# Performance work log

Measured on AMD Instinct MI355X. Metric: run time of the kernel, lower is better.

The kernel has to match this reference:

```python
import jax, jax.numpy as jnp
import numpy as np

D_MODEL = 256
N_HEADS = 8
D_HEAD = D_MODEL // N_HEADS
B = 65536
LN_EPS = 1e-5


def setup_inputs() -> dict:
    key = jax.random.key(0)
    ks = jax.random.split(key, 6)
    s = 1.0 / np.sqrt(D_MODEL)
    x = jax.random.normal(ks[0], (B, D_MODEL), dtype=jnp.float32)
    Wq = jax.random.normal(ks[1], (D_MODEL, D_MODEL), dtype=jnp.float32) * s
    Wk = jax.random.normal(ks[2], (D_MODEL, D_MODEL), dtype=jnp.float32) * s
    Wv = jax.random.normal(ks[3], (D_MODEL, D_MODEL), dtype=jnp.float32) * s
    Wout = jax.random.normal(ks[4], (D_MODEL, D_MODEL), dtype=jnp.float32) * s
    b_out = jnp.zeros((D_MODEL,), dtype=jnp.float32)
    # L initialized to identity per head (matches nn.init.eye_) plus tiny noise
    L = jnp.broadcast_to(jnp.eye(D_HEAD, dtype=jnp.float32), (N_HEADS, D_HEAD, D_HEAD)) \
        + 0.01 * jax.random.normal(ks[5], (N_HEADS, D_HEAD, D_HEAD), dtype=jnp.float32)
    gamma = jnp.ones((D_MODEL,), dtype=jnp.float32)
    beta = jnp.zeros((D_MODEL,), dtype=jnp.float32)
    return {"x": x, "Wq": Wq, "Wk": Wk, "Wv": Wv, "Wout": Wout,
            "b_out": b_out, "L": L, "gamma": gamma, "beta": beta}


def reference(x, Wq, Wk, Wv, Wout, b_out, L, gamma, beta):
    b = x.shape[0]
    # projections; view as [B, H, d_head]
    Q = (x @ Wq).reshape(b, N_HEADS, D_HEAD)
    K = (x @ Wk).reshape(b, N_HEADS, D_HEAD)
    V = (x @ Wv).reshape(b, N_HEADS, D_HEAD)
    # pairwise head differences: [B, Hq, Hk, d_head]
    diff = Q[:, :, None, :] - K[:, None, :, :]
    # per-key-head learned metric transform: L indexed by key head
    diff_t = jnp.einsum('bqkd,kdf->bqkf', diff, L)
    sq_dist = jnp.sum(diff_t * diff_t, axis=-1)            # [B, Hq, Hk]
    attn = jax.nn.softmax(-sq_dist / jnp.sqrt(jnp.float32(D_HEAD)), axis=2)
    out = jnp.einsum('bqk,bkd->bqd', attn, V).reshape(b, D_MODEL)
    out = out @ Wout + b_out
    h = out + x
    # LayerNorm over last dim
    mu = jnp.mean(h, axis=-1, keepdims=True)
    var = jnp.mean((h - mu) ** 2, axis=-1, keepdims=True)
    return (h - mu) * jax.lax.rsqrt(var + LN_EPS) * gamma + beta
```

## Files before the change

kernel.cpp:

```cpp
#include <hip/hip_runtime.h>


typedef __bf16 bf16x8 __attribute__((ext_vector_type(8)));
typedef float  f32x4  __attribute__((ext_vector_type(4)));
typedef int    i32x4  __attribute__((ext_vector_type(4)));
typedef unsigned short u16;

__device__ __forceinline__ float bf2f(u16 u){
  unsigned int x = ((unsigned int)u) << 16;
  return __builtin_bit_cast(float, x);
}
__device__ __forceinline__ u16 f2bf(float f){
  unsigned int u = __builtin_bit_cast(unsigned int, f);
  u += 0x7FFFu + ((u >> 16) & 1u);
  return (u16)(u >> 16);
}
__device__ __forceinline__ unsigned int pk2(float lo, float hi){
  return ((unsigned int)f2bf(hi) << 16) | (unsigned int)f2bf(lo);
}
__device__ __forceinline__ bf16x8 ldfrag(const u16* p){
  return __builtin_bit_cast(bf16x8, *(const i32x4*)p);
}

#define LROW 264
#define HROW 260

__global__ __launch_bounds__(256) void geo_prep(
    const float* __restrict__ Wq, const float* __restrict__ Wk,
    const float* __restrict__ Wv, const float* __restrict__ Wout,
    const float* __restrict__ L, u16* __restrict__ ws)
{
  u16* Wd    = ws;
  u16* WvT   = ws + 524288;
  u16* WoutT = ws + 589824;
  const int b = blockIdx.x, t = threadIdx.x;

  if (b < 64){
    const int q = b >> 3, k = b & 7;
    __shared__ float dwb[256][33];
    __shared__ float Lk[32][33];
    for (int i = 0; i < 4; ++i){
      int idx = t + i*256;
      Lk[idx >> 5][idx & 31] = L[k*1024 + idx];
    }
    {
      const int c = t;
      const float* wqp = Wq + c*256 + q*32;
      const float* wkp = Wk + c*256 + k*32;
      #pragma unroll
      for (int j = 0; j < 8; ++j){
        f32x4 a  = *(const f32x4*)(wqp + j*4);
        f32x4 bb = *(const f32x4*)(wkp + j*4);
        #pragma unroll
        for (int p = 0; p < 4; ++p) dwb[c][j*4 + p] = a[p] - bb[p];
      }
    }
    __syncthreads();
    const int c = t;
    float wreg[32];
    #pragma unroll
    for (int d = 0; d < 32; ++d) wreg[d] = dwb[c][d];
    for (int f = 0; f < 32; ++f){
      float s = 0.f;
      #pragma unroll
      for (int d = 0; d < 32; ++d) s = fmaf(wreg[d], Lk[d][f], s);
      Wd[(size_t)(q*256 + k*32 + f)*256 + c] = f2bf(s);
    }
  } else {
    const int bb  = b - 64;
    const float* src = (bb < 16) ? Wv  : Wout;
    u16*         dst = (bb < 16) ? WvT : WoutT;
    const int tile = bb & 15;
    const int tr = tile >> 2, tc = tile & 3;
    __shared__ float tlf[64][68];
    {
      const int row = t >> 2, cs = (t & 3)*16;
      #pragma unroll
      for (int j = 0; j < 4; ++j){
        f32x4 v = *(const f32x4*)(src + (size_t)(tr*64 + row)*256 + tc*64 + cs + j*4);
        #pragma unroll
        for (int p = 0; p < 4; ++p) tlf[row][cs + j*4 + p] = v[p];
      }
    }
    __syncthreads();
    {
      const int n = t >> 2, cs = (t & 3)*16;
      float us[16];
      #pragma unroll
      for (int j = 0; j < 16; ++j) us[j] = tlf[cs + j][n];
      #pragma unroll
      for (int h = 0; h < 2; ++h){
        i32x4 o;
        #pragma unroll
        for (int p = 0; p < 4; ++p)
          o[p] = (int)pk2(us[h*8 + 2*p], us[h*8 + 2*p + 1]);
        *(i32x4*)(dst + (size_t)(tc*64 + n)*256 + tr*64 + cs + h*8) = o;
      }
    }
  }
}

__global__ __launch_bounds__(512) void geo_fused(
    const float* __restrict__ x,   const u16* __restrict__ Wd,
    const u16* __restrict__ WvT,   const u16* __restrict__ WoutT,
    const float* __restrict__ b_out, const float* __restrict__ gamma,
    const float* __restrict__ beta,  float* __restrict__ out)
{
  __shared__ __align__(16) char pool[125952];
  u16  (*xs)[LROW]   = (u16 (*)[LROW])(pool);
  u16  (*Vs)[LROW]   = (u16 (*)[LROW])(pool + 33792);
  u16  (*ao)[LROW]   = (u16 (*)[LROW])(pool + 67584);
  float (*sqs)[8][12] = (float (*)[8][12])(pool + 101376);
  float (*hs)[HROW]  = (float (*)[HROW])(pool);

  const int t    = threadIdx.x;
  const int lane = t & 63;
  const int w    = t >> 6;
  const int l15  = lane & 15;
  const int quad = lane >> 4;
  const long rowbase = (long)blockIdx.x * 64;

  {
    const int r  = t >> 3;
    const int c0 = (t & 7) * 32;
    const float* src = x + (rowbase + r)*256 + c0;
    unsigned int words[16];
    #pragma unroll
    for (int j = 0; j < 8; ++j){
      f32x4 v = *(const f32x4*)(src + j*4);
      words[j*2    ] = pk2(v[0], v[1]);
      words[j*2 + 1] = pk2(v[2], v[3]);
    }
    #pragma unroll
    for (int qd = 0; qd < 4; ++qd){
      i32x4 o;
      #pragma unroll
      for (int p = 0; p < 4; ++p) o[p] = (int)words[qd*4 + p];
      *(i32x4*)&xs[r][c0 + qd*8] = o;
    }
  }
  __syncthreads();

  {
    f32x4 acc[4][2];
    #pragma unroll
    for (int mt = 0; mt < 4; ++mt)
      #pragma unroll
      for (int nt = 0; nt < 2; ++nt) acc[mt][nt] = f32x4{0.f,0.f,0.f,0.f};
    #pragma unroll
    for (int kk = 0; kk < 8; ++kk){
      const int c0 = kk*32 + quad*8;
      bf16x8 a[4], bfr[2];
      #pragma unroll
      for (int mt = 0; mt < 4; ++mt) a[mt] = ldfrag(&xs[mt*16 + l15][c0]);
      #pragma unroll
      for (int nt = 0; nt < 2; ++nt){
        const int n = w*32 + nt*16 + l15;
        bfr[nt] = __builtin_bit_cast(bf16x8, *(const i32x4*)(WvT + (size_t)n*256 + c0));
      }
      #pragma unroll
      for (int mt = 0; mt < 4; ++mt)
        #pragma unroll
        for (int nt = 0; nt < 2; ++nt)
          acc[mt][nt] = __builtin_amdgcn_mfma_f32_16x16x32_bf16(a[mt], bfr[nt], acc[mt][nt], 0, 0, 0);
    }
    #pragma unroll
    for (int mt = 0; mt < 4; ++mt)
      #pragma unroll
      for (int nt = 0; nt < 2; ++nt){
        const int col = w*32 + nt*16 + l15;
        #pragma unroll
        for (int reg = 0; reg < 4; ++reg)
          Vs[mt*16 + quad*4 + reg][col] = f2bf(acc[mt][nt][reg]);
      }
  }

  {
    #pragma unroll
    for (int kp = 0; kp < 4; ++kp){
      f32x4 acc[2][2][4];
      #pragma unroll
      for (int k2 = 0; k2 < 2; ++k2)
        #pragma unroll
        for (int mt = 0; mt < 2; ++mt)
          #pragma unroll
          for (int nt = 0; nt < 4; ++nt) acc[k2][mt][nt] = f32x4{0.f,0.f,0.f,0.f};
      #pragma unroll
      for (int kk = 0; kk < 8; ++kk){
        const int c0 = kk*32 + quad*8;
        bf16x8 bfr[4];
        #pragma unroll
        for (int nt = 0; nt < 4; ++nt) bfr[nt] = ldfrag(&xs[nt*16 + l15][c0]);
        bf16x8 a[2][2];
        #pragma unroll
        for (int k2 = 0; k2 < 2; ++k2)
          #pragma unroll
          for (int mt = 0; mt < 2; ++mt){
            const int m = w*256 + (kp*2 + k2)*32 + mt*16 + l15;
            a[k2][mt] = __builtin_bit_cast(bf16x8, *(const i32x4*)(Wd + (size_t)m*256 + c0));
          }
        #pragma unroll
        for (int k2 = 0; k2 < 2; ++k2)
          #pragma unroll
          for (int mt = 0; mt < 2; ++mt)
            #pragma unroll
            for (int nt = 0; nt < 4; ++nt)
              acc[k2][mt][nt] = __builtin_amdgcn_mfma_f32_16x16x32_bf16(a[k2][mt], bfr[nt], acc[k2][mt][nt], 0, 0, 0);
      }
      #pragma unroll
      for (int k2 = 0; k2 < 2; ++k2){
        const int k = kp*2 + k2;
        #pragma unroll
        for (int nt = 0; nt < 4; ++nt){
          float s = 0.f;
          #pragma unroll
          for (int mt = 0; mt < 2; ++mt)
            #pragma unroll
            for (int reg = 0; reg < 4; ++reg){
              float d = acc[k2][mt][nt][reg];
              s = fmaf(d, d, s);
            }
          s += __shfl_xor(s, 16);
          s += __shfl_xor(s, 32);
          if (quad == 0) sqs[nt*16 + l15][w][k] = s;
        }
      }
    }
  }
  __syncthreads();

  {
    const int r = t >> 3, q = t & 7;
    float lg[8];
    #pragma unroll
    for (int k = 0; k < 8; ++k) lg[k] = sqs[r][q][k] * -0.17677669529663687f;
    float mx = lg[0];
    #pragma unroll
    for (int k = 1; k < 8; ++k) mx = fmaxf(mx, lg[k]);
    float e[8], sum = 0.f;
    #pragma unroll
    for (int k = 0; k < 8; ++k){ e[k] = __expf(lg[k] - mx); sum += e[k]; }
    const float inv = 1.0f / sum;
    #pragma unroll
    for (int k = 0; k < 8; ++k) e[k] *= inv;

    #pragma unroll
    for (int dc = 0; dc < 4; ++dc){
      const int d0 = dc*8;
      float o[8] = {0.f,0.f,0.f,0.f,0.f,0.f,0.f,0.f};
      #pragma unroll
      for (int k = 0; k < 8; ++k){
        i32x4 v = *(const i32x4*)&Vs[r][k*32 + d0];
        const float a = e[k];
        #pragma unroll
        for (int p = 0; p < 4; ++p){
          unsigned int u = (unsigned int)v[p];
          o[2*p    ] = fmaf(a, __builtin_bit_cast(float, u << 16),          o[2*p    ]);
          o[2*p + 1] = fmaf(a, __builtin_bit_cast(float, u & 0xFFFF0000u),  o[2*p + 1]);
        }
      }
      i32x4 pkv;
      #pragma unroll
      for (int p = 0; p < 4; ++p)
        pkv[p] = (int)pk2(o[2*p], o[2*p + 1]);
      *(i32x4*)&ao[r][q*32 + d0] = pkv;
    }
  }
  __syncthreads();

  {
    f32x4 acc[4][2];
    #pragma unroll
    for (int mt = 0; mt < 4; ++mt)
      #pragma unroll
      for (int nt = 0; nt < 2; ++nt) acc[mt][nt] = f32x4{0.f,0.f,0.f,0.f};
    #pragma unroll
    for (int kk = 0; kk < 8; ++kk){
      const int c0 = kk*32 + quad*8;
      bf16x8 a[4], bfr[2];
      #pragma unroll
      for (int mt = 0; mt < 4; ++mt) a[mt] = ldfrag(&ao[mt*16 + l15][c0]);
      #pragma unroll
      for (int nt = 0; nt < 2; ++nt){
        const int n = w*32 + nt*16 + l15;
        bfr[nt] = __builtin_bit_cast(bf16x8, *(const i32x4*)(WoutT + (size_t)n*256 + c0));
      }
      #pragma unroll
      for (int mt = 0; mt < 4; ++mt)
        #pragma unroll
        for (int nt = 0; nt < 2; ++nt)
          acc[mt][nt] = __builtin_amdgcn_mfma_f32_16x16x32_bf16(a[mt], bfr[nt], acc[mt][nt], 0, 0, 0);
    }
    #pragma unroll
    for (int nt = 0; nt < 2; ++nt){
      const int col = w*32 + nt*16 + l15;
      const float bo = b_out[col];
      #pragma unroll
      for (int mt = 0; mt < 4; ++mt)
        #pragma unroll
        for (int reg = 0; reg < 4; ++reg){
          const int row = mt*16 + quad*4 + reg;
          hs[row][col] = acc[mt][nt][reg] + bo + x[(rowbase + row)*256 + col];
        }
    }
  }
  __syncthreads();

  {
    #pragma unroll
    for (int rr = 0; rr < 8; ++rr){
      const int r = w*8 + rr;
      const int c = lane*4;
      f32x4 hv = *(const f32x4*)&hs[r][c];
      float s  = hv[0] + hv[1] + hv[2] + hv[3];
      float s2 = hv[0]*hv[0] + hv[1]*hv[1] + hv[2]*hv[2] + hv[3]*hv[3];
      #pragma unroll
      for (int off = 1; off < 64; off <<= 1){
        s  += __shfl_xor(s,  off);
        s2 += __shfl_xor(s2, off);
      }
      const float mu  = s  * (1.0f/256.0f);
      const float var = s2 * (1.0f/256.0f) - mu*mu;
      const float rs  = rsqrtf(var + 1e-5f);
      f32x4 gv = *(const f32x4*)(gamma + c);
      f32x4 bv = *(const f32x4*)(beta  + c);
      f32x4 y;
      y[0] = (hv[0] - mu)*rs*gv[0] + bv[0];
      y[1] = (hv[1] - mu)*rs*gv[1] + bv[1];
      y[2] = (hv[2] - mu)*rs*gv[2] + bv[2];
      y[3] = (hv[3] - mu)*rs*gv[3] + bv[3];
      *(f32x4*)(out + (rowbase + r)*256 + c) = y;
    }
  }
}

extern "C" void kernel_launch(void* const* d_in, const int* in_sizes, int n_in,
                              void* d_out, int out_size, void* d_ws, size_t ws_size,
                              hipStream_t stream)
{
  const float* x     = (const float*)d_in[0];
  const float* Wq    = (const float*)d_in[1];
  const float* Wk    = (const float*)d_in[2];
  const float* Wv    = (const float*)d_in[3];
  const float* Wout  = (const float*)d_in[4];
  const float* b_out = (const float*)d_in[5];
  const float* L     = (const float*)d_in[6];
  const float* gamma = (const float*)d_in[7];
  const float* beta  = (const float*)d_in[8];
  u16* ws = (u16*)d_ws;

  geo_prep<<<96, 256, 0, stream>>>(Wq, Wk, Wv, Wout, L, ws);
  geo_fused<<<1024, 512, 0, stream>>>(x, ws, ws + 524288, ws + 589824,
                                      b_out, gamma, beta, (float*)d_out);
}
```

Before: 300.0 us.

## Shrink LDS footprint via fp16 logits, bf16 residual staging, and buffer aliasing

Cuts shared memory from about 123KB to 74KB by storing the scaled attention logits as fp16, staging the output-projection result as bf16 instead of fp32, and aliasing the attention-output buffer onto the x buffer. The residual add with x moves into the LayerNorm pass and reads x straight from global memory with vector loads. The softmax/V mixing is remapped so each wave handles its own query head across 64 rows, and the kernel declares a min-blocks hint of 4. The aim is more resident blocks per CU to hide latency. The cost is extra rounding on the logits and on the pre-residual output.

```diff
diff --git a/kernel.cpp b/kernel.cpp
--- a/kernel.cpp
+++ b/kernel.cpp
@@ -2,8 +2,10 @@
 
 
 typedef __bf16 bf16x8 __attribute__((ext_vector_type(8)));
+typedef _Float16 f16x8 __attribute__((ext_vector_type(8)));
 typedef float  f32x4  __attribute__((ext_vector_type(4)));
 typedef int    i32x4  __attribute__((ext_vector_type(4)));
+typedef int    i32x2  __attribute__((ext_vector_type(2)));
 typedef unsigned short u16;
 
 __device__ __forceinline__ float bf2f(u16 u){
@@ -23,7 +25,6 @@
 }
 
 #define LROW 264
-#define HROW 260
 
 __global__ __launch_bounds__(256) void geo_prep(
     const float* __restrict__ Wq, const float* __restrict__ Wk,
@@ -100,18 +101,18 @@
   }
 }
 
-__global__ __launch_bounds__(512) void geo_fused(
+__global__ __launch_bounds__(512, 4) void geo_fused(
     const float* __restrict__ x,   const u16* __restrict__ Wd,
     const u16* __restrict__ WvT,   const u16* __restrict__ WoutT,
     const float* __restrict__ b_out, const float* __restrict__ gamma,
     const float* __restrict__ beta,  float* __restrict__ out)
 {
-  __shared__ __align__(16) char pool[125952];
-  u16  (*xs)[LROW]   = (u16 (*)[LROW])(pool);
-  u16  (*Vs)[LROW]   = (u16 (*)[LROW])(pool + 33792);
-  u16  (*ao)[LROW]   = (u16 (*)[LROW])(pool + 67584);
-  float (*sqs)[8][12] = (float (*)[8][12])(pool + 101376);
-  float (*hs)[HROW]  = (float (*)[HROW])(pool);
+  __shared__ __align__(16) char pool[75776];
+  u16  (*xs)[LROW] = (u16 (*)[LROW])(pool);
+  u16  (*Vs)[LROW] = (u16 (*)[LROW])(pool + 33792);
+  u16  (*ao)[LROW] = (u16 (*)[LROW])(pool);
+  u16  (*hs)[256]  = (u16 (*)[256])(pool + 33792);
+  _Float16* sqh    = (_Float16*)(pool + 67584);
 
   const int t    = threadIdx.x;
   const int lane = t & 63;
@@ -222,7 +223,9 @@
             }
           s += __shfl_xor(s, 16);
           s += __shfl_xor(s, 32);
-          if (quad == 0) sqs[nt*16 + l15][w][k] = s;
+          if (quad == 0)
+            sqh[w*512 + (nt*16 + l15)*8 + k] =
+                (_Float16)(s * -0.17677669529663687f);
         }
       }
     }
@@ -230,28 +233,25 @@
   __syncthreads();
 
   {
-    const int r = t >> 3, q = t & 7;
-    float lg[8];
-    #pragma unroll
-    for (int k = 0; k < 8; ++k) lg[k] = sqs[r][q][k] * -0.17677669529663687f;
-    float mx = lg[0];
-    #pragma unroll
-    for (int k = 1; k < 8; ++k) mx = fmaxf(mx, lg[k]);
-    float e[8], sum = 0.f;
-    #pragma unroll
-    for (int k = 0; k < 8; ++k){ e[k] = __expf(lg[k] - mx); sum += e[k]; }
-    const float inv = 1.0f / sum;
-    #pragma unroll
-    for (int k = 0; k < 8; ++k) e[k] *= inv;
-
-    #pragma unroll
-    for (int dc = 0; dc < 4; ++dc){
-      const int d0 = dc*8;
+    #pragma unroll
+    for (int nt = 0; nt < 4; ++nt){
+      const int r = nt*16 + l15;
+      f16x8 lgh = __builtin_bit_cast(f16x8, *(const i32x4*)&sqh[w*512 + r*8]);
+      float lg[8];
+      #pragma unroll
+      for (int k = 0; k < 8; ++k) lg[k] = (float)lgh[k];
+      float mx = lg[0];
+      #pragma unroll
+      for (int k = 1; k < 8; ++k) mx = fmaxf(mx, lg[k]);
+      float e[8], sum = 0.f;
+      #pragma unroll
+      for (int k = 0; k < 8; ++k){ e[k] = __expf(lg[k] - mx); sum += e[k]; }
+      const float inv = 1.0f / sum;
       float o[8] = {0.f,0.f,0.f,0.f,0.f,0.f,0.f,0.f};
       #pragma unroll
       for (int k = 0; k < 8; ++k){
-        i32x4 v = *(const i32x4*)&Vs[r][k*32 + d0];
-        const float a = e[k];
+        i32x4 v = *(const i32x4*)&Vs[r][k*32 + quad*8];
+        const float a = e[k] * inv;
         #pragma unroll
         for (int p = 0; p < 4; ++p){
           unsigned int u = (unsigned int)v[p];
@@ -261,9 +261,8 @@
       }
       i32x4 pkv;
       #pragma unroll
-      for (int p = 0; p < 4; ++p)
-        pkv[p] = (int)pk2(o[2*p], o[2*p + 1]);
-      *(i32x4*)&ao[r][q*32 + d0] = pkv;
+      for (int p = 0; p < 4; ++p) pkv[p] = (int)pk2(o[2*p], o[2*p + 1]);
+      *(i32x4*)&ao[r][w*32 + quad*8] = pkv;
     }
   }
   __syncthreads();
@@ -300,7 +299,7 @@
         #pragma unroll
         for (int reg = 0; reg < 4; ++reg){
           const int row = mt*16 + quad*4 + reg;
-          hs[row][col] = acc[mt][nt][reg] + bo + x[(rowbase + row)*256 + col];
+          hs[row][col] = f2bf(acc[mt][nt][reg] + bo);
         }
     }
   }
@@ -311,7 +310,14 @@
     for (int rr = 0; rr < 8; ++rr){
       const int r = w*8 + rr;
       const int c = lane*4;
-      f32x4 hv = *(const f32x4*)&hs[r][c];
+      i32x2 hv2 = *(const i32x2*)&hs[r][c];
+      f32x4 xv  = *(const f32x4*)(x + (rowbase + r)*256 + c);
+      unsigned int u0 = (unsigned int)hv2[0], u1 = (unsigned int)hv2[1];
+      f32x4 hv;
+      hv[0] = __builtin_bit_cast(float, u0 << 16)         + xv[0];
+      hv[1] = __builtin_bit_cast(float, u0 & 0xFFFF0000u) + xv[1];
+      hv[2] = __builtin_bit_cast(float, u1 << 16)         + xv[2];
+      hv[3] = __builtin_bit_cast(float, u1 & 0xFFFF0000u) + xv[3];
       float s  = hv[0] + hv[1] + hv[2] + hv[3];
       float s2 = hv[0]*hv[0] + hv[1]*hv[1] + hv[2]*hv[2] + hv[3]*hv[3];
       #pragma unroll
```

Result: slower. 307.3 us (+2.4%).
